# Optimization experiments

Measured on AMD Instinct MI355X. Metric: run time of the kernel, lower is better.

The kernel has to match this reference:

```python
import jax, jax.numpy as jnp
import numpy as np

N_TOKENS = 1024
D = 768
MAX_SPAN_W = 30
FEAT = 20
FFNN = 1000
TOP_RATIO = 0.4
MAX_TOP_ANT = 50
NUM_GENRES = 7
MAX_TRAIN_SENTS = 11
NEG = -1e9
SPAN_DIM = 2 * D + FEAT + D          # start + end + width feat + head-attn emb = 2324
PAIR_DIM = 3 * SPAN_DIM + 4 * FEAT   # 7052


def _ffnn(x, w1, b1, w2, b2):
    # Linear -> ReLU -> Linear (dropout = identity at eval)
    return jax.nn.relu(x @ w1 + b1) @ w2 + b2


def bucket_distance(d):
    # coref-hoi log-space distance bucketing into 10 buckets
    logspace = jnp.floor(jnp.log2(jnp.maximum(d, 1).astype(jnp.float32))).astype(d.dtype) + 3
    return jnp.clip(jnp.where(d <= 4, d, logspace), 0, 9)


def setup_inputs() -> dict:
    key = jax.random.key(0)
    ks = iter(jax.random.split(key, 40))
    rn = lambda shape: jax.random.normal(next(ks), shape, jnp.float32) * 0.02
    return dict(
        token_embs=jax.random.normal(next(ks), (N_TOKENS, D), jnp.float32),
        speaker_ids=jax.random.randint(next(ks), (N_TOKENS,), 0, 10),
        sentence_map=jnp.sort(jax.random.randint(next(ks), (N_TOKENS,), 0, 64)),
        token_seg_ids=jnp.sort(jax.random.randint(next(ks), (N_TOKENS,), 0, 8)),
        genre=3,
        emb_span_width=rn((MAX_SPAN_W, FEAT)),
        emb_span_width_prior=rn((MAX_SPAN_W, FEAT)),
        w_ment_attn=rn((D, 1)), b_ment_attn=jnp.zeros((1,), jnp.float32),
        w_span1=rn((SPAN_DIM, FFNN)), b_span1=jnp.zeros((FFNN,), jnp.float32),
        w_span2=rn((FFNN, 1)), b_span2=jnp.zeros((1,), jnp.float32),
        w_width1=rn((FEAT, FFNN)), b_width1=jnp.zeros((FFNN,), jnp.float32),
        w_width2=rn((FFNN, 1)), b_width2=jnp.zeros((1,), jnp.float32),
        w_biaffine=rn((SPAN_DIM, SPAN_DIM + 1)),
        emb_ant_dist_prior=rn((10, FEAT)),
        w_antdist=rn((FEAT, 1)), b_antdist=jnp.zeros((1,), jnp.float32),
        emb_same_speaker=rn((2, FEAT)),
        emb_genre=rn((NUM_GENRES, FEAT)),
        emb_seg_dist=rn((MAX_TRAIN_SENTS, FEAT)),
        emb_top_ant_dist=rn((10, FEAT)),
        w_pair1=rn((PAIR_DIM, FFNN)), b_pair1=jnp.zeros((FFNN,), jnp.float32),
        w_pair2=rn((FFNN, 1)), b_pair2=jnp.zeros((1,), jnp.float32),
    )


def _forward(token_embs, speaker_ids, sentence_map, token_seg_ids, genre,
             emb_span_width, emb_span_width_prior, w_ment_attn, b_ment_attn,
             w_span1, b_span1, w_span2, b_span2,
             w_width1, b_width1, w_width2, b_width2,
             w_biaffine, emb_ant_dist_prior, w_antdist, b_antdist,
             emb_same_speaker, emb_genre, emb_seg_dist, emb_top_ant_dist,
             w_pair1, b_pair1, w_pair2, b_pair2):
    n = token_embs.shape[0]
    widths = jnp.arange(MAX_SPAN_W)
    starts = jnp.repeat(jnp.arange(n)[:, None], MAX_SPAN_W, axis=1)   # [n, W]
    ends = starts + widths
    ends_c = jnp.minimum(ends, n - 1)
    # candidate valid if it fits in the doc and stays within one sentence
    valid = (ends < n) & (sentence_map[starts] == sentence_map[ends_c])
    starts = starts.reshape(-1)
    ends = ends_c.reshape(-1)
    valid = valid.reshape(-1)
    width_idx = jnp.broadcast_to(widths, (n, MAX_SPAN_W)).reshape(-1)  # [n*W]

    # --- candidate span embeddings ---
    start_emb = token_embs[starts]          # [C, D]
    end_emb = token_embs[ends]              # [C, D]
    width_emb = emb_span_width[width_idx]   # [C, FEAT]
    token_attn = (token_embs @ w_ment_attn + b_ment_attn)[:, 0]        # [n]
    doc = jnp.arange(n)
    span_tok_mask = (starts[:, None] <= doc) & (doc <= ends[:, None])  # [C, n]
    attn = jax.nn.softmax(jnp.where(span_tok_mask, token_attn[None, :], NEG), axis=-1)
    head_emb = attn @ token_embs            # [C, D]
    cand_emb = jnp.concatenate([start_emb, end_emb, width_emb, head_emb], axis=-1)

    # --- mention scores (span emb score + width prior score) ---
    ment = _ffnn(cand_emb, w_span1, b_span1, w_span2, b_span2)[:, 0]
    width_prior = _ffnn(emb_span_width_prior, w_width1, b_width1, w_width2, b_width2)[:, 0]
    ment = jnp.where(valid, ment + width_prior[width_idx], NEG)

    # --- top-span pruning (padded candidates carry -inf scores) ---
    n_top = int(TOP_RATIO * n)
    _, top_idx = jax.lax.top_k(ment, n_top)
    top_idx = jnp.sort(top_idx)             # flat idx = start*W + width -> (start, end) order
    top_starts = starts[top_idx]
    top_ends = ends[top_idx]
    top_emb = cand_emb[top_idx]             # [T, SPAN_DIM]
    top_ment = ment[top_idx]

    # --- coarse antecedent scoring: mention sums + biaffine + distance prior ---
    y = jnp.concatenate([top_emb, jnp.ones((n_top, 1), top_emb.dtype)], axis=-1)  # bias_y
    biaff = jnp.einsum('xi,ij,yj->xy', top_emb, w_biaffine, y)
    offsets = jnp.arange(n_top)[:, None] - jnp.arange(n_top)[None, :]
    ant_mask = offsets >= 1
    dist_prior = (emb_ant_dist_prior @ w_antdist + b_antdist)[:, 0]    # [10]
    coarse = (top_ment[:, None] + top_ment[None, :] + biaff
              + jnp.where(ant_mask, 0.0, NEG)
              + dist_prior[bucket_distance(jnp.maximum(offsets, 0))])

    # --- top-k antecedent pruning ---
    k = min(MAX_TOP_ANT, n_top)
    top_ant_coarse, top_ant_idx = jax.lax.top_k(coarse, k)             # [T, k]
    top_ant_mask = jnp.take_along_axis(ant_mask, top_ant_idx, axis=1)
    top_ant_offsets = jnp.take_along_axis(offsets, top_ant_idx, axis=1)

    # --- pairwise features ---
    top_speaker = speaker_ids[top_starts]
    same_speaker = (top_speaker[:, None] == top_speaker[top_ant_idx]).astype(jnp.int32)
    same_speaker_emb = emb_same_speaker[same_speaker]                  # [T, k, FEAT]
    genre_emb = jnp.broadcast_to(emb_genre[genre], (n_top, k, FEAT))
    top_seg = token_seg_ids[top_starts]
    seg_dist = jnp.clip(top_seg[:, None] - top_seg[top_ant_idx], 0, MAX_TRAIN_SENTS - 1)
    seg_dist_emb = emb_seg_dist[seg_dist]
    ant_dist_emb = emb_top_ant_dist[bucket_distance(jnp.maximum(top_ant_offsets, 0))]
    feat = jnp.concatenate([same_speaker_emb, genre_emb, seg_dist_emb, ant_dist_emb], axis=-1)

    # --- fine (slow) coref scoring over pair embeddings ---
    tgt = top_emb[top_ant_idx]                                         # [T, k, SPAN_DIM]
    src = jnp.broadcast_to(top_emb[:, None], tgt.shape)
    pair = jnp.concatenate([src, tgt, src * tgt, feat], axis=-1)       # [T, k, PAIR_DIM]
    slow = _ffnn(pair, w_pair1, b_pair1, w_pair2, b_pair2)[..., 0]
    ant_scores = jnp.where(top_ant_mask, slow + top_ant_coarse, NEG)
    final = jnp.concatenate([jnp.zeros((n_top, 1), ant_scores.dtype), ant_scores], axis=-1)
    return top_starts, top_ends, top_ant_idx, final


def reference(token_embs, speaker_ids, sentence_map, token_seg_ids, genre,
              emb_span_width, emb_span_width_prior, w_ment_attn, b_ment_attn,
              w_span1, b_span1, w_span2, b_span2,
              w_width1, b_width1, w_width2, b_width2,
              w_biaffine, emb_ant_dist_prior, w_antdist, b_antdist,
              emb_same_speaker, emb_genre, emb_seg_dist, emb_top_ant_dist,
              w_pair1, b_pair1, w_pair2, b_pair2):
    return _forward(token_embs, speaker_ids, sentence_map, token_seg_ids, genre,
                    emb_span_width, emb_span_width_prior, w_ment_attn, b_ment_attn,
                    w_span1, b_span1, w_span2, b_span2,
                    w_width1, b_width1, w_width2, b_width2,
                    w_biaffine, emb_ant_dist_prior, w_antdist, b_antdist,
                    emb_same_speaker, emb_genre, emb_seg_dist, emb_top_ant_dist,
                    w_pair1, b_pair1, w_pair2, b_pair2)
```

## Files before the change

### kernel.cpp

```cpp
#include <hip/hip_runtime.h>
#include <math.h>

#define NEGF (-1e9f)

constexpr int NT = 1024;
constexpr int D  = 768;
constexpr int SW = 30;
constexpr int NC = NT * SW;
constexpr int FT = 20;
constexpr int FF = 1000;
constexpr int TOPN = 409;
constexpr int KA = 50;
constexpr int SD = 2 * D + FT + D;
constexpr int MP = TOPN * KA;
constexpr int KP = 2336;
constexpr int NKT = KP / 32;

typedef short short8 __attribute__((ext_vector_type(8)));
typedef float f32x4 __attribute__((ext_vector_type(4)));

constexpr size_t al8(size_t x) { return (x + 7) & ~(size_t)7; }
constexpr size_t O_TOKATT = 0;
constexpr size_t O_WPS    = al8(O_TOKATT + 1024);
constexpr size_t O_DPR    = al8(O_WPS + 32);
constexpr size_t O_MENT   = al8(O_DPR + 16);
constexpr size_t O_TIDX   = al8(O_MENT + NC);
constexpr size_t O_TST    = al8(O_TIDX + 512);
constexpr size_t O_TEN    = al8(O_TST + 512);
constexpr size_t O_TME    = al8(O_TEN + 512);
constexpr size_t O_TEMB   = al8(O_TME + 512);
constexpr size_t O_TMPB   = al8(O_TEMB + (size_t)TOPN * SD);
constexpr size_t O_COARSE = al8(O_TMPB + (size_t)TOPN * (SD + 1));
constexpr size_t O_ANTI   = al8(O_COARSE + (size_t)TOPN * TOPN);
constexpr size_t O_ANTC   = al8(O_ANTI + 20480);
constexpr size_t O_SLOW   = al8(O_ANTC + 20480);
constexpr size_t O_E      = al8(O_SLOW + 20480);
constexpr size_t O_E2W    = al8(O_E + (size_t)NT * 3072);
constexpr size_t O_PALL   = al8(O_E2W + 30 * 1024);
constexpr size_t O_HST    = al8(O_PALL + 24 * 1024);
constexpr size_t O_TEMBH  = al8(O_HST + (size_t)512 * 2048);
constexpr size_t O_W1ST   = al8(O_TEMBH + (size_t)512 * KP / 2);
constexpr size_t O_W1P    = al8(O_W1ST + (size_t)2048 * KP / 2);

__device__ __forceinline__ unsigned int f2sort(float f) {
    unsigned int u = __float_as_uint(f);
    return (u & 0x80000000u) ? ~u : (u | 0x80000000u);
}
__device__ __forceinline__ int bucket_dist(int d) {
    if (d <= 4) return d;
    return min(34 - __clz(d), 9);
}
__device__ __forceinline__ unsigned short f2bf(float f) {
    unsigned u = __float_as_uint(f);
    unsigned r = (u + 0x7fffu + ((u >> 16) & 1u)) >> 16;
    return (unsigned short)r;
}
__device__ __forceinline__ float bf2f(unsigned short s) {
    return __uint_as_float(((unsigned)s) << 16);
}

__global__ void k_init(const float* b_p2, float* slow) {
    int i = blockIdx.x * 256 + threadIdx.x;
    if (i < MP) slow[i] = b_p2[0];
}

__global__ void k_zero(float* p, int n) {
    int i = blockIdx.x * 256 + threadIdx.x;
    if (i < n) p[i] = 0.f;
}
__global__ void k_zero4(float* p, int n4) {
    int i = blockIdx.x * 256 + threadIdx.x;
    if (i < n4) ((float4*)p)[i] = make_float4(0.f, 0.f, 0.f, 0.f);
}

__global__ void k_tokatt(const float* emb, const float* w, const float* b, float* out) {
    int wave = threadIdx.x >> 6, lane = threadIdx.x & 63;
    int tok = blockIdx.x * 4 + wave;
    float s = 0.f;
    for (int d = lane; d < D; d += 64) s += emb[tok * D + d] * w[d];
    for (int o = 32; o; o >>= 1) s += __shfl_down(s, o);
    if (lane == 0) out[tok] = s + b[0];
}

__global__ void k_widthps(const float* e, const float* w1, const float* b1,
                          const float* w2, const float* b2, float* out) {
    int wi = blockIdx.x;
    float acc = 0.f;
    for (int n = threadIdx.x; n < FF; n += 256) {
        float h = b1[n];
        for (int f = 0; f < FT; ++f) h += e[wi * FT + f] * w1[f * FF + n];
        acc += fmaxf(h, 0.f) * w2[n];
    }
    __shared__ float red[256];
    red[threadIdx.x] = acc; __syncthreads();
    for (int s = 128; s; s >>= 1) {
        if (threadIdx.x < s) red[threadIdx.x] += red[threadIdx.x + s];
        __syncthreads();
    }
    if (threadIdx.x == 0) out[wi] = red[0] + b2[0];
}

__global__ void k_distpr(const float* e, const float* w, const float* b, float* out) {
    int d = threadIdx.x;
    if (d < 10) {
        float s = b[0];
        for (int f = 0; f < FT; ++f) s += e[d * FT + f] * w[f];
        out[d] = s;
    }
}

__global__ void k_e2w(const float* ew, const float* w1, float* e2w) {
    int idx = blockIdx.x * 256 + threadIdx.x;
    if (idx >= 30 * 1024) return;
    int wd = idx >> 10, n = idx & 1023;
    float s = 0.f;
    if (n < FF) for (int f = 0; f < FT; ++f) s += ew[wd * FT + f] * w1[(2 * D + f) * FF + n];
    e2w[idx] = s;
}

__global__ void k_prep_pall(const float* w1, const float* b1, const int* genre,
                            const float* e_same, const float* e_genre,
                            const float* e_seg, const float* e_antd, float* pall) {
    int idx = blockIdx.x * 256 + threadIdx.x;
    if (idx >= 24 * 1024) return;
    int r = idx >> 10, n = idx & 1023;
    float s = 0.f;
    if (n < FF) {
        const float* tab; int foff;
        if (r < 2)       { tab = e_same + r * FT;          foff = 0; }
        else if (r == 2) { tab = e_genre + genre[0] * FT;  foff = FT; s = b1[n]; }
        else if (r < 14) { tab = e_seg + (r - 3) * FT;     foff = 2 * FT; }
        else             { tab = e_antd + (r - 14) * FT;   foff = 3 * FT; }
        for (int f = 0; f < FT; ++f) s += tab[f] * w1[(size_t)(3 * SD + foff + f) * FF + n];
    }
    pall[idx] = s;
}

__global__ void k_cvt_temb(const float* temb, unsigned short* tembh) {
    int idx = blockIdx.x * 256 + threadIdx.x;
    if (idx >= 512 * KP) return;
    int t = idx / KP, k = idx % KP;
    float v = (t < TOPN && k < SD) ? temb[(size_t)t * SD + k] : 0.f;
    tembh[idx] = f2bf(v);
}

__global__ void k_cvt_w1(const float* w1, unsigned short* dst, int mode) {
    __shared__ float tile[32][33];
    int kp0 = blockIdx.x * 32;
    int r0  = blockIdx.y * 32;
    int tx = threadIdx.x & 31, ty = threadIdx.x >> 5;
    for (int i = 0; i < 4; ++i) {
        int r = r0 + tx, kp = kp0 + ty + i * 8;
        int c, ro;
        if (mode == 0) { c = r & 1023; ro = (r >> 10) * SD; }
        else           { c = r;        ro = 2 * SD; }
        float v = (c < FF && kp < SD) ? w1[(size_t)(ro + kp) * FF + c] : 0.f;
        tile[ty + i * 8][tx] = v;
    }
    __syncthreads();
    for (int i = 0; i < 4; ++i) {
        int r = r0 + ty + i * 8, kp = kp0 + tx;
        dst[(size_t)r * KP + kp] = f2bf(tile[tx][ty + i * 8]);
    }
}

__global__ __launch_bounds__(256) void k_ment(
    const float* __restrict__ E, const float* __restrict__ e2w,
    const float* __restrict__ tokatt, const int* __restrict__ sentmap,
    const float* __restrict__ b1, const float* __restrict__ w2,
    const float* __restrict__ wps, const float* __restrict__ b_s2, float* ment) {
    int st = blockIdx.x;
    __shared__ float earr[32];
    __shared__ int vmask[32];
    __shared__ float swred[4][32];
    int tid = threadIdx.x;
    if (tid < SW) {
        int en = st + tid;
        bool ok = en < NT;
        earr[tid] = ok ? expf(tokatt[en]) : 0.f;
        vmask[tid] = ok && (sentmap[st] == sentmap[en]);
    }
    __syncthreads();
    int n4 = tid * 4;
    bool act = n4 < FF;
    float4 Es = {0,0,0,0}, B1 = {0,0,0,0}, W2 = {0,0,0,0};
    if (act) {
        Es = *(const float4*)(E + (size_t)st * 3072 + n4);
        B1 = *(const float4*)(b1 + n4);
        W2 = *(const float4*)(w2 + n4);
    }
    float Ux = 0, Uy = 0, Uz = 0, Uw = 0, S = 0.f;
    float part[SW];
    #pragma unroll
    for (int wd = 0; wd < SW; ++wd) {
        int en = st + wd;
        float p = 0.f;
        if (en < NT) {
            float e = earr[wd]; S += e;
            if (act) {
                float4 Eh = *(const float4*)(E + (size_t)en * 3072 + 2048 + n4);
                Ux += e * Eh.x; Uy += e * Eh.y; Uz += e * Eh.z; Uw += e * Eh.w;
                if (vmask[wd]) {
                    float inv = 1.f / S;
                    float4 Ee = *(const float4*)(E + (size_t)en * 3072 + 1024 + n4);
                    float4 Ww = *(const float4*)(e2w + wd * 1024 + n4);
                    float vx = Es.x + Ee.x + Ww.x + B1.x + Ux * inv;
                    float vy = Es.y + Ee.y + Ww.y + B1.y + Uy * inv;
                    float vz = Es.z + Ee.z + Ww.z + B1.z + Uz * inv;
                    float vw = Es.w + Ee.w + Ww.w + B1.w + Uw * inv;
                    p = fmaxf(vx, 0.f) * W2.x + fmaxf(vy, 0.f) * W2.y
                      + fmaxf(vz, 0.f) * W2.z + fmaxf(vw, 0.f) * W2.w;
                }
            }
        }
        part[wd] = p;
    }
    int lane = tid & 63, wv = tid >> 6;
    #pragma unroll
    for (int wd = 0; wd < SW; ++wd) {
        float r = part[wd];
        r += __shfl_xor(r, 1);  r += __shfl_xor(r, 2);  r += __shfl_xor(r, 4);
        r += __shfl_xor(r, 8);  r += __shfl_xor(r, 16); r += __shfl_xor(r, 32);
        if (lane == 0) swred[wv][wd] = r;
    }
    __syncthreads();
    if (tid < SW) {
        float tot = swred[0][tid] + swred[1][tid] + swred[2][tid] + swred[3][tid];
        ment[st * SW + tid] = vmask[tid] ? (tot + wps[tid] + b_s2[0]) : NEGF;
    }
}

__global__ __launch_bounds__(1024) void k_topk(const float* ment, int* topidx) {
    __shared__ unsigned int hist[256];
    __shared__ unsigned int sc[1024];
    __shared__ unsigned int sh_prefix, sh_needed, sh_run, sh_base2, sh_rune;
    int tid = threadIdx.x;
    if (tid == 0) { sh_prefix = 0; sh_needed = TOPN; }
    for (int r = 3; r >= 0; --r) {
        if (tid < 256) hist[tid] = 0;
        __syncthreads();
        unsigned int pref = sh_prefix;
        for (int c = tid; c < NC; c += 1024) {
            unsigned int u = f2sort(ment[c]);
            bool match = (r == 3) || ((u >> ((r + 1) * 8)) == pref);
            if (match) atomicAdd(&hist[(u >> (r * 8)) & 255u], 1u);
        }
        __syncthreads();
        if (tid == 0) {
            unsigned int need = sh_needed, cum = 0; int sel = 0;
            for (int b = 255; b >= 0; --b) {
                if (cum + hist[b] >= need) { sel = b; sh_needed = need - cum; break; }
                cum += hist[b];
            }
            sh_prefix = (sh_prefix << 8) | (unsigned int)sel;
        }
        __syncthreads();
    }
    unsigned int kth = sh_prefix;
    unsigned int quota = sh_needed;
    if (tid == 0) sh_run = 0;
    __syncthreads();
    for (int base = 0; base < NC; base += 1024) {
        int c = base + tid;
        unsigned int u = f2sort(ment[c]);
        unsigned int flag = (u > kth) ? 1u : 0u;
        sc[tid] = flag; __syncthreads();
        for (int off = 1; off < 1024; off <<= 1) {
            unsigned int v = (tid >= off) ? sc[tid - off] : 0u;
            __syncthreads();
            sc[tid] += v;
            __syncthreads();
        }
        if (flag) topidx[sh_run + sc[tid] - 1] = c;
        unsigned int tot = sc[1023];
        __syncthreads();
        if (tid == 0) sh_run += tot;
        __syncthreads();
    }
    if (tid == 0) { sh_base2 = sh_run; sh_rune = 0; }
    __syncthreads();
    for (int base = 0; base < NC; base += 1024) {
        int c = base + tid;
        unsigned int u = f2sort(ment[c]);
        unsigned int flag = (u == kth) ? 1u : 0u;
        sc[tid] = flag; __syncthreads();
        for (int off = 1; off < 1024; off <<= 1) {
            unsigned int v = (tid >= off) ? sc[tid - off] : 0u;
            __syncthreads();
            sc[tid] += v;
            __syncthreads();
        }
        if (flag && (sh_rune + sc[tid] - 1) < quota)
            topidx[sh_base2 + sh_rune + sc[tid] - 1] = c;
        unsigned int tot = sc[1023];
        __syncthreads();
        if (tid == 0) sh_rune += tot;
        __syncthreads();
    }
    __shared__ int arr[512];
    if (tid < 512) arr[tid] = (tid < TOPN) ? topidx[tid] : 0x7fffffff;
    __syncthreads();
    for (int k = 2; k <= 512; k <<= 1) {
        for (int j = k >> 1; j > 0; j >>= 1) {
            if (tid < 512) {
                int i = tid, p = i ^ j;
                if (p > i) {
                    bool asc = ((i & k) == 0);
                    int a = arr[i], b = arr[p];
                    if ((a > b) == asc) { arr[i] = b; arr[p] = a; }
                }
            }
            __syncthreads();
        }
    }
    if (tid < TOPN) topidx[tid] = arr[tid];
}

__global__ void k_gather(const float* emb, const float* wemb, const float* tokatt,
                         const float* ment, const int* topidx,
                         int* tst, int* ten, float* tme, float* temb,
                         float* out_s, float* out_e) {
    int t = blockIdx.x;
    int c = topidx[t];
    int st = c / SW, wd = c % SW;
    int en = min(st + wd, NT - 1);
    int len = en - st + 1;
    __shared__ float p[32];
    if (threadIdx.x == 0) {
        float m = -1e30f;
        for (int j = 0; j < len; ++j) m = fmaxf(m, tokatt[st + j]);
        float s = 0.f;
        for (int j = 0; j < len; ++j) { p[j] = expf(tokatt[st + j] - m); s += p[j]; }
        float inv = 1.f / s;
        for (int j = 0; j < len; ++j) p[j] *= inv;
        tst[t] = st; ten[t] = en; tme[t] = ment[c];
        out_s[t] = (float)st; out_e[t] = (float)en;
    }
    __syncthreads();
    for (int k = threadIdx.x; k < SD; k += 256) {
        float val;
        if (k < D) val = emb[st * D + k];
        else if (k < 2 * D) val = emb[en * D + (k - D)];
        else if (k < 2 * D + FT) val = wemb[wd * FT + (k - 2 * D)];
        else {
            int d = k - 2 * D - FT;
            float a = 0.f;
            for (int j = 0; j < len; ++j) a += p[j] * emb[(st + j) * D + d];
            val = a;
        }
        temb[(size_t)t * SD + k] = val;
    }
}

template<int BT>
__global__ __launch_bounds__(256) void k_sgemm(
    const float* __restrict__ A, const float* __restrict__ B, float* __restrict__ C,
    int M, int N, int K, int lda, int ldb, int ldc, int kch) {
    int m0 = blockIdx.x * 64, n0 = blockIdx.y * 64;
    int kbeg = blockIdx.z * kch;
    int kend = min(K, kbeg + kch);
    __shared__ float As[32][68], Bs[32][68];
    int tid = threadIdx.x, tx = tid & 15, ty = tid >> 4;
    float acc[4][4] = {};
    float ra[8], rb[8];

    auto loadA = [&](int k0) {
        #pragma unroll
        for (int i = 0; i < 8; ++i) {
            int lid = tid + i * 256;
            int rr = lid >> 5, kk = lid & 31;
            int m = m0 + rr, k = k0 + kk;
            ra[i] = (m < M && k < kend) ? A[(size_t)m * lda + k] : 0.f;
        }
    };
    auto loadB = [&](int k0) {
        #pragma unroll
        for (int i = 0; i < 8; ++i) {
            int lid = tid + i * 256;
            if (BT) {
                int y = lid >> 5, kk = lid & 31;
                int n = n0 + y, k = k0 + kk;
                rb[i] = (n < N && k < kend) ? B[(size_t)n * ldb + k] : 0.f;
            } else {
                int rr = lid >> 6, nn = lid & 63;
                int k = k0 + rr, n = n0 + nn;
                rb[i] = (k < kend && n < N) ? B[(size_t)k * ldb + n] : 0.f;
            }
        }
    };

    loadA(kbeg); loadB(kbeg);
    for (int k0 = kbeg; k0 < kend; k0 += 32) {
        __syncthreads();
        float sa[8], sb[8];
        #pragma unroll
        for (int i = 0; i < 8; ++i) { sa[i] = ra[i]; sb[i] = rb[i]; }
        #pragma unroll
        for (int i = 0; i < 8; ++i) {
            int lid = tid + i * 256;
            As[lid & 31][lid >> 5] = sa[i];
            if (BT) Bs[lid & 31][lid >> 5] = sb[i];
            else    Bs[lid >> 6][lid & 63] = sb[i];
        }
        __syncthreads();
        if (k0 + 32 < kend) { loadA(k0 + 32); loadB(k0 + 32); }
        #pragma unroll
        for (int kk = 0; kk < 32; ++kk) {
            float4 a = *(const float4*)&As[kk][ty * 4];
            float4 b = *(const float4*)&Bs[kk][tx * 4];
            acc[0][0] += a.x * b.x; acc[0][1] += a.x * b.y; acc[0][2] += a.x * b.z; acc[0][3] += a.x * b.w;
            acc[1][0] += a.y * b.x; acc[1][1] += a.y * b.y; acc[1][2] += a.y * b.z; acc[1][3] += a.y * b.w;
            acc[2][0] += a.z * b.x; acc[2][1] += a.z * b.y; acc[2][2] += a.z * b.z; acc[2][3] += a.z * b.w;
            acc[3][0] += a.w * b.x; acc[3][1] += a.w * b.y; acc[3][2] += a.w * b.z; acc[3][3] += a.w * b.w;
        }
    }
    #pragma unroll
    for (int i = 0; i < 4; ++i)
        #pragma unroll
        for (int j = 0; j < 4; ++j) {
            int m = m0 + ty * 4 + i, n = n0 + tx * 4 + j;
            if (m < M && n < N) atomicAdd(&C[(size_t)m * ldc + n], acc[i][j]);
        }
}

__global__ void k_initco(const float* tmpb, const float* tme, const float* dpr, float* coarse) {
    int idx = blockIdx.x * 256 + threadIdx.x;
    if (idx >= TOPN * TOPN) return;
    int x = idx / TOPN, y = idx - x * TOPN;
    int off = x - y;
    coarse[idx] = tmpb[(size_t)x * (SD + 1) + SD] + tme[x] + tme[y]
                + ((off >= 1) ? 0.f : NEGF) + dpr[bucket_dist(max(off, 0))];
}

__global__ __launch_bounds__(256) void k_topant(const float* coarse, int* anti,
                                                float* antc, float* out_ai) {
    int x = blockIdx.x;
    int tid = threadIdx.x;
    __shared__ float vals[512];
    __shared__ unsigned long long red[256];
    vals[tid] = (tid < TOPN) ? coarse[(size_t)x * TOPN + tid] : -INFINITY;
    vals[tid + 256] = (tid + 256 < TOPN) ? coarse[(size_t)x * TOPN + tid + 256] : -INFINITY;
    __syncthreads();
    for (int j = 0; j < KA; ++j) {
        unsigned long long best = 0ull;
        for (int h = 0; h < 2; ++h) {
            int y = tid + h * 256;
            unsigned long long p = ((unsigned long long)f2sort(vals[y]) << 32)
                                 | (unsigned long long)(0xFFFFFFFFu - (unsigned int)y);
            if (p > best) best = p;
        }
        red[tid] = best; __syncthreads();
        for (int s = 128; s; s >>= 1) {
            if (tid < s) { if (red[tid + s] > red[tid]) red[tid] = red[tid + s]; }
            __syncthreads();
        }
        if (tid == 0) {
            unsigned long long r = red[0];
            int y = (int)(0xFFFFFFFFu - (unsigned int)(r & 0xFFFFFFFFu));
            anti[x * KA + j] = y;
            antc[x * KA + j] = vals[y];
            out_ai[x * KA + j] = (float)y;
            vals[y] = -INFINITY;
        }
        __syncthreads();
    }
}

template<int MODE>
__global__ __launch_bounds__(256) void k_mm(
    const unsigned short* __restrict__ tembh, const unsigned short* __restrict__ w1t,
    const int* __restrict__ anti, const int* __restrict__ tstv,
    const int* __restrict__ spk, const int* __restrict__ seg,
    const float* __restrict__ Hst, const float* __restrict__ Pall,
    const float* __restrict__ w2, float* __restrict__ outp) {
    __shared__ unsigned short As[128 * 40];
    __shared__ unsigned short Bs[128 * 40];
    const int tid = threadIdx.x;
    const int m0 = blockIdx.x * 128, n0 = blockIdx.y * 128;
    const int l = tid & 63, wv = tid >> 6, wr = wv >> 1, wc = wv & 1;
    const int r = tid >> 1, h = tid & 1;

    const unsigned short *pa0, *pa1;
    bool za = false;
    if (MODE == 0) {
        pa0 = tembh + (size_t)(m0 + r) * KP + h * 16;
        pa1 = pa0;
    } else {
        int m = m0 + r;
        if (m < MP) {
            int t = m / KA; int a = anti[m];
            pa0 = tembh + (size_t)t * KP + h * 16;
            pa1 = tembh + (size_t)a * KP + h * 16;
        } else { za = true; pa0 = tembh; pa1 = tembh; }
    }
    const unsigned short* pb = w1t + (size_t)(n0 + r) * KP + h * 16;
    unsigned short* awr = As + r * 40 + h * 16;
    unsigned short* bwr = Bs + r * 40 + h * 16;

    short8 ra0, ra1, rb0, rb1, rc0, rc1;
    ra0 = *(const short8*)(pa0); ra1 = *(const short8*)(pa0 + 8);
    if (MODE == 1) { rb0 = *(const short8*)(pa1); rb1 = *(const short8*)(pa1 + 8); }
    rc0 = *(const short8*)(pb);  rc1 = *(const short8*)(pb + 8);

    f32x4 acc[4][4];
    #pragma unroll
    for (int i = 0; i < 4; ++i)
        #pragma unroll
        for (int j = 0; j < 4; ++j) acc[i][j] = (f32x4){0.f, 0.f, 0.f, 0.f};

    for (int kt = 0; kt < NKT; ++kt) {
        __syncthreads();
        short8 wa0, wa1;
        if (MODE == 0) { wa0 = ra0; wa1 = ra1; }
        else {
            #pragma unroll
            for (int e = 0; e < 8; ++e) {
                float x0 = bf2f((unsigned short)ra0[e]) * bf2f((unsigned short)rb0[e]);
                float x1 = bf2f((unsigned short)ra1[e]) * bf2f((unsigned short)rb1[e]);
                wa0[e] = za ? (short)0 : (short)f2bf(x0);
                wa1[e] = za ? (short)0 : (short)f2bf(x1);
            }
        }
        *(short8*)(awr) = wa0; *(short8*)(awr + 8) = wa1;
        *(short8*)(bwr) = rc0; *(short8*)(bwr + 8) = rc1;
        __syncthreads();
        if (kt + 1 < NKT) {
            int ko = (kt + 1) * 32;
            ra0 = *(const short8*)(pa0 + ko); ra1 = *(const short8*)(pa0 + ko + 8);
            if (MODE == 1) { rb0 = *(const short8*)(pa1 + ko); rb1 = *(const short8*)(pa1 + ko + 8); }
            rc0 = *(const short8*)(pb + ko);  rc1 = *(const short8*)(pb + ko + 8);
        }
        short8 af[4], bfr[4];
        #pragma unroll
        for (int mf = 0; mf < 4; ++mf)
            af[mf] = *(const short8*)(As + (wr * 64 + mf * 16 + (l & 15)) * 40 + (l >> 4) * 8);
        #pragma unroll
        for (int nf = 0; nf < 4; ++nf)
            bfr[nf] = *(const short8*)(Bs + (wc * 64 + nf * 16 + (l & 15)) * 40 + (l >> 4) * 8);
        #pragma unroll
        for (int mf = 0; mf < 4; ++mf)
            #pragma unroll
            for (int nf = 0; nf < 4; ++nf)
                acc[mf][nf] = __builtin_amdgcn_mfma_f32_16x16x32_bf16(af[mf], bfr[nf], acc[mf][nf], 0, 0, 0);
    }

    if (MODE == 0) {
        #pragma unroll
        for (int mf = 0; mf < 4; ++mf)
            #pragma unroll
            for (int nf = 0; nf < 4; ++nf)
                #pragma unroll
                for (int rg = 0; rg < 4; ++rg) {
                    int m = m0 + wr * 64 + mf * 16 + (l >> 4) * 4 + rg;
                    int n = n0 + wc * 64 + nf * 16 + (l & 15);
                    outp[(size_t)m * 2048 + n] = acc[mf][nf][rg];
                }
    } else {
        #pragma unroll
        for (int mf = 0; mf < 4; ++mf) {
            #pragma unroll
            for (int rg = 0; rg < 4; ++rg) {
                int m = m0 + wr * 64 + mf * 16 + (l >> 4) * 4 + rg;
                float ps = 0.f;
                if (m < MP) {
                    int t = m / KA; int a = anti[m];
                    int u1 = tstv[t], u2 = tstv[a];
                    const float* rs = Hst + (size_t)t * 2048;
                    const float* rt = Hst + (size_t)a * 2048 + 1024;
                    const float* q1 = Pall + ((spk[u1] == spk[u2]) ? 1 : 0) * 1024;
                    const float* q2 = Pall + 2 * 1024;
                    int sdv = seg[u1] - seg[u2]; sdv = min(max(sdv, 0), 10);
                    const float* q3 = Pall + (3 + sdv) * 1024;
                    const float* q4 = Pall + (14 + bucket_dist(max(t - a, 0))) * 1024;
                    #pragma unroll
                    for (int nf = 0; nf < 4; ++nf) {
                        int n = n0 + wc * 64 + nf * 16 + (l & 15);
                        if (n < FF) {
                            float v = acc[mf][nf][rg] + rs[n] + rt[n] + q1[n] + q2[n] + q3[n] + q4[n];
                            ps += fmaxf(v, 0.f) * w2[n];
                        }
                    }
                }
                ps += __shfl_xor(ps, 1); ps += __shfl_xor(ps, 2);
                ps += __shfl_xor(ps, 4); ps += __shfl_xor(ps, 8);
                if ((l & 15) == 0 && m < MP) atomicAdd(&outp[m], ps);
            }
        }
    }
}

__global__ void k_final(const int* anti, const float* slow, const float* antc, float* out_f) {
    int t = blockIdx.x, j = threadIdx.x;
    if (j < KA) {
        int a = anti[t * KA + j];
        float sc = (a < t) ? (slow[t * KA + j] + antc[t * KA + j]) : NEGF;
        out_f[t * (KA + 1) + 1 + j] = sc;
    }
    if (j == KA) out_f[t * (KA + 1)] = 0.f;
}

extern "C" void kernel_launch(void* const* d_in, const int* in_sizes, int n_in,
                              void* d_out, int out_size, void* d_ws, size_t ws_size,
                              hipStream_t stream) {
    const float* token_embs = (const float*)d_in[0];
    const int*   speaker    = (const int*)d_in[1];
    const int*   sentmap    = (const int*)d_in[2];
    const int*   segids     = (const int*)d_in[3];
    const int*   genre      = (const int*)d_in[4];
    const float* e_width    = (const float*)d_in[5];
    const float* e_width_pr = (const float*)d_in[6];
    const float* w_matt     = (const float*)d_in[7];
    const float* b_matt     = (const float*)d_in[8];
    const float* w_s1       = (const float*)d_in[9];
    const float* b_s1       = (const float*)d_in[10];
    const float* w_s2       = (const float*)d_in[11];
    const float* b_s2       = (const float*)d_in[12];
    const float* w_w1       = (const float*)d_in[13];
    const float* b_w1       = (const float*)d_in[14];
    const float* w_w2       = (const float*)d_in[15];
    const float* b_w2       = (const float*)d_in[16];
    const float* w_bi       = (const float*)d_in[17];
    const float* e_adp      = (const float*)d_in[18];
    const float* w_ad       = (const float*)d_in[19];
    const float* b_ad       = (const float*)d_in[20];
    const float* e_same     = (const float*)d_in[21];
    const float* e_genre    = (const float*)d_in[22];
    const float* e_seg      = (const float*)d_in[23];
    const float* e_antd     = (const float*)d_in[24];
    const float* w_p1       = (const float*)d_in[25];
    const float* b_p1       = (const float*)d_in[26];
    const float* w_p2       = (const float*)d_in[27];
    const float* b_p2       = (const float*)d_in[28];

    float* F = (float*)d_ws;
    float* tokatt = F + O_TOKATT;
    float* wps    = F + O_WPS;
    float* dpr    = F + O_DPR;
    float* ment   = F + O_MENT;
    int*   tidx   = (int*)(F + O_TIDX);
    int*   tst    = (int*)(F + O_TST);
    int*   ten    = (int*)(F + O_TEN);
    float* tme    = F + O_TME;
    float* temb   = F + O_TEMB;
    float* tmpb   = F + O_TMPB;
    float* coarse = F + O_COARSE;
    int*   anti   = (int*)(F + O_ANTI);
    float* antc   = F + O_ANTC;
    float* slow   = F + O_SLOW;
    float* E      = F + O_E;
    float* e2w    = F + O_E2W;
    float* pall   = F + O_PALL;
    float* hst    = F + O_HST;
    unsigned short* tembh = (unsigned short*)(F + O_TEMBH);
    unsigned short* w1st  = (unsigned short*)(F + O_W1ST);
    unsigned short* w1p   = (unsigned short*)(F + O_W1P);

    float* out    = (float*)d_out;
    float* out_s  = out;
    float* out_e  = out + TOPN;
    float* out_ai = out + 2 * TOPN;
    float* out_f  = out + 2 * TOPN + MP;

    k_init<<<(MP + 255) / 256, 256, 0, stream>>>(b_p2, slow);
    k_cvt_w1<<<dim3(NKT, 64), 256, 0, stream>>>(w_p1, w1st, 0);
    k_cvt_w1<<<dim3(NKT, 32), 256, 0, stream>>>(w_p1, w1p, 1);
    k_prep_pall<<<(24 * 1024 + 255) / 256, 256, 0, stream>>>(w_p1, b_p1, genre,
                                                             e_same, e_genre, e_seg, e_antd, pall);
    k_tokatt<<<NT / 4, 256, 0, stream>>>(token_embs, w_matt, b_matt, tokatt);
    k_widthps<<<SW, 256, 0, stream>>>(e_width_pr, w_w1, b_w1, w_w2, b_w2, wps);
    k_distpr<<<1, 64, 0, stream>>>(e_adp, w_ad, b_ad, dpr);

    k_zero4<<<(NT * 3072 / 4 + 255) / 256, 256, 0, stream>>>(E, NT * 3072 / 4);
    {
        dim3 g(NT / 64, (FF + 63) / 64, 2);
        k_sgemm<0><<<g, 256, 0, stream>>>(token_embs, w_s1,                 E,        NT, FF, D, D, FF, 3072, 384);
        k_sgemm<0><<<g, 256, 0, stream>>>(token_embs, w_s1 + D * FF,        E + 1024, NT, FF, D, D, FF, 3072, 384);
        k_sgemm<0><<<g, 256, 0, stream>>>(token_embs, w_s1 + (2*D+FT) * FF, E + 2048, NT, FF, D, D, FF, 3072, 384);
    }
    k_e2w<<<(30 * 1024 + 255) / 256, 256, 0, stream>>>(e_width, w_s1, e2w);

    k_ment<<<NT, 256, 0, stream>>>(E, e2w, tokatt, sentmap, b_s1, w_s2, wps, b_s2, ment);
    k_topk<<<1, 1024, 0, stream>>>(ment, tidx);
    k_gather<<<TOPN, 256, 0, stream>>>(token_embs, e_width, tokatt, ment, tidx,
                                       tst, ten, tme, temb, out_s, out_e);
    k_cvt_temb<<<(512 * KP + 255) / 256, 256, 0, stream>>>(temb, tembh);

    k_zero<<<(TOPN * (SD + 1) + 255) / 256, 256, 0, stream>>>(tmpb, TOPN * (SD + 1));
    {
        dim3 g((TOPN + 63) / 64, (SD + 1 + 63) / 64, 4);
        k_sgemm<0><<<g, 256, 0, stream>>>(temb, w_bi, tmpb, TOPN, SD + 1, SD, SD, SD + 1, SD + 1, 608);
    }
    k_initco<<<(TOPN * TOPN + 255) / 256, 256, 0, stream>>>(tmpb, tme, dpr, coarse);
    {
        dim3 g((TOPN + 63) / 64, (TOPN + 63) / 64, 8);
        k_sgemm<1><<<g, 256, 0, stream>>>(tmpb, temb, coarse, TOPN, TOPN, SD, SD + 1, SD, TOPN, 320);
    }
    k_topant<<<TOPN, 256, 0, stream>>>(coarse, anti, antc, out_ai);

    k_mm<0><<<dim3(4, 16), 256, 0, stream>>>(tembh, w1st, anti, tst, speaker, segids,
                                             hst, pall, w_p2, hst);
    k_mm<1><<<dim3(160, 8), 256, 0, stream>>>(tembh, w1p, anti, tst, speaker, segids,
                                              hst, pall, w_p2, slow);
    k_final<<<TOPN, 64, 0, stream>>>(anti, slow, antc, out_f);
}
```

Measured before the change: 1.100 ms.

## Precompute pair products, speed up topk compaction and per-warp antecedent selection

When the workspace is large enough, a separate kernel materializes the bf16 elementwise products of each span and its antecedent into a buffer, so the pair GEMM streams a plain A matrix instead of doing gathers and multiplies inside its K loop. The grid is transposed so blocks that share an A tile run close together. Top-k compaction now uses a single blocked prefix scan plus a merge by binary search instead of a chunked scan and a bitonic sort. Antecedent top-50 selection uses one wavefront per row with register shuffles instead of shared-memory reductions. The product buffer costs a large extra write and read of memory, and the old fused path is kept as a fallback.

```diff
diff --git a/kernel.cpp b/kernel.cpp
--- a/kernel.cpp
+++ b/kernel.cpp
@@ -13,8 +13,10 @@
 constexpr int KA = 50;
 constexpr int SD = 2 * D + FT + D;
 constexpr int MP = TOPN * KA;
+constexpr int MPP = 20480;
 constexpr int KP = 2336;
 constexpr int NKT = KP / 32;
+constexpr int CHPR = KP / 8;
 
 typedef short short8 __attribute__((ext_vector_type(8)));
 typedef float f32x4 __attribute__((ext_vector_type(4)));
@@ -34,17 +36,23 @@
 constexpr size_t O_ANTI   = al8(O_COARSE + (size_t)TOPN * TOPN);
 constexpr size_t O_ANTC   = al8(O_ANTI + 20480);
 constexpr size_t O_SLOW   = al8(O_ANTC + 20480);
-constexpr size_t O_E      = al8(O_SLOW + 20480);
-constexpr size_t O_E2W    = al8(O_E + (size_t)NT * 3072);
-constexpr size_t O_PALL   = al8(O_E2W + 30 * 1024);
+constexpr size_t O_PALL   = al8(O_SLOW + 20480);
 constexpr size_t O_HST    = al8(O_PALL + 24 * 1024);
 constexpr size_t O_TEMBH  = al8(O_HST + (size_t)512 * 2048);
 constexpr size_t O_W1ST   = al8(O_TEMBH + (size_t)512 * KP / 2);
 constexpr size_t O_W1P    = al8(O_W1ST + (size_t)2048 * KP / 2);
+constexpr size_t O_E      = al8(O_W1P + (size_t)1024 * KP / 2);
+constexpr size_t O_E2W    = O_E + (size_t)NT * 3072;
+constexpr size_t PRODH_F  = (size_t)MPP * KP / 2;
+constexpr size_t O_END_BIG   = O_E + PRODH_F;
+constexpr size_t O_END_SMALL = O_E2W + 30 * 1024;
 
 __device__ __forceinline__ unsigned int f2sort(float f) {
     unsigned int u = __float_as_uint(f);
     return (u & 0x80000000u) ? ~u : (u | 0x80000000u);
+}
+__device__ __forceinline__ float sort2f(unsigned int s) {
+    return __uint_as_float((s & 0x80000000u) ? (s & 0x7FFFFFFFu) : ~s);
 }
 __device__ __forceinline__ int bucket_dist(int d) {
     if (d <= 4) return d;
@@ -162,6 +170,23 @@
         int r = r0 + ty + i * 8, kp = kp0 + tx;
         dst[(size_t)r * KP + kp] = f2bf(tile[tx][ty + i * 8]);
     }
+}
+
+__global__ void k_prod(const unsigned short* __restrict__ tembh, const int* __restrict__ anti,
+                       unsigned short* __restrict__ prodh) {
+    int idx = blockIdx.x * 256 + threadIdx.x;
+    if (idx >= MP * CHPR) return;
+    int m = idx / CHPR;
+    int ch = idx - m * CHPR;
+    int t = m / KA;
+    int a = anti[m];
+    short8 x = *(const short8*)(tembh + (size_t)t * KP + ch * 8);
+    short8 y = *(const short8*)(tembh + (size_t)a * KP + ch * 8);
+    short8 o;
+    #pragma unroll
+    for (int e = 0; e < 8; ++e)
+        o[e] = (short)f2bf(bf2f((unsigned short)x[e]) * bf2f((unsigned short)y[e]));
+    *(short8*)(prodh + (size_t)m * KP + ch * 8) = o;
 }
 
 __global__ __launch_bounds__(256) void k_ment(
@@ -233,87 +258,79 @@
 __global__ __launch_bounds__(1024) void k_topk(const float* ment, int* topidx) {
     __shared__ unsigned int hist[256];
     __shared__ unsigned int sc[1024];
-    __shared__ unsigned int sh_prefix, sh_needed, sh_run, sh_base2, sh_rune;
+    __shared__ int lA[512], lB[512];
+    __shared__ unsigned int sh_prefix, sh_needed;
     int tid = threadIdx.x;
     if (tid == 0) { sh_prefix = 0; sh_needed = TOPN; }
-    for (int r = 3; r >= 0; --r) {
+    for (int rd = 3; rd >= 0; --rd) {
         if (tid < 256) hist[tid] = 0;
         __syncthreads();
-        unsigned int pref = sh_prefix;
+        unsigned pref = sh_prefix;
         for (int c = tid; c < NC; c += 1024) {
-            unsigned int u = f2sort(ment[c]);
-            bool match = (r == 3) || ((u >> ((r + 1) * 8)) == pref);
-            if (match) atomicAdd(&hist[(u >> (r * 8)) & 255u], 1u);
+            unsigned u = f2sort(ment[c]);
+            bool match = (rd == 3) || ((u >> ((rd + 1) * 8)) == pref);
+            if (match) atomicAdd(&hist[(u >> (rd * 8)) & 255u], 1u);
         }
         __syncthreads();
         if (tid == 0) {
-            unsigned int need = sh_needed, cum = 0; int sel = 0;
+            unsigned need = sh_needed, cum = 0; int sel = 0;
             for (int b = 255; b >= 0; --b) {
                 if (cum + hist[b] >= need) { sel = b; sh_needed = need - cum; break; }
                 cum += hist[b];
             }
-            sh_prefix = (sh_prefix << 8) | (unsigned int)sel;
-        }
-        __syncthreads();
-    }
-    unsigned int kth = sh_prefix;
-    unsigned int quota = sh_needed;
-    if (tid == 0) sh_run = 0;
+            sh_prefix = (sh_prefix << 8) | (unsigned)sel;
+        }
+        __syncthreads();
+    }
+    unsigned kth = sh_prefix;
+    int quota = (int)sh_needed;
+    int base = tid * 30;
+    int cgt = 0, ceq = 0;
+    for (int j = 0; j < 30; ++j) {
+        unsigned uu = f2sort(ment[base + j]);
+        cgt += (uu > kth); ceq += (uu == kth);
+    }
+    sc[tid] = (unsigned)cgt; __syncthreads();
+    for (int off = 1; off < 1024; off <<= 1) {
+        unsigned v = (tid >= off) ? sc[tid - off] : 0u;
+        __syncthreads(); sc[tid] += v; __syncthreads();
+    }
+    int egt = (int)sc[tid] - cgt;
+    int nA = (int)sc[1023];
+    int p = egt;
+    for (int j = 0; j < 30; ++j) {
+        int c = base + j;
+        if (f2sort(ment[c]) > kth) lA[p++] = c;
+    }
     __syncthreads();
-    for (int base = 0; base < NC; base += 1024) {
-        int c = base + tid;
-        unsigned int u = f2sort(ment[c]);
-        unsigned int flag = (u > kth) ? 1u : 0u;
-        sc[tid] = flag; __syncthreads();
-        for (int off = 1; off < 1024; off <<= 1) {
-            unsigned int v = (tid >= off) ? sc[tid - off] : 0u;
-            __syncthreads();
-            sc[tid] += v;
-            __syncthreads();
-        }
-        if (flag) topidx[sh_run + sc[tid] - 1] = c;
-        unsigned int tot = sc[1023];
-        __syncthreads();
-        if (tid == 0) sh_run += tot;
-        __syncthreads();
-    }
-    if (tid == 0) { sh_base2 = sh_run; sh_rune = 0; }
+    sc[tid] = (unsigned)ceq; __syncthreads();
+    for (int off = 1; off < 1024; off <<= 1) {
+        unsigned v = (tid >= off) ? sc[tid - off] : 0u;
+        __syncthreads(); sc[tid] += v; __syncthreads();
+    }
+    int eeq = (int)sc[tid] - ceq;
+    p = eeq;
+    for (int j = 0; j < 30; ++j) {
+        int c = base + j;
+        if (f2sort(ment[c]) == kth) { if (p < quota) lB[p] = c; p++; }
+    }
     __syncthreads();
-    for (int base = 0; base < NC; base += 1024) {
-        int c = base + tid;
-        unsigned int u = f2sort(ment[c]);
-        unsigned int flag = (u == kth) ? 1u : 0u;
-        sc[tid] = flag; __syncthreads();
-        for (int off = 1; off < 1024; off <<= 1) {
-            unsigned int v = (tid >= off) ? sc[tid - off] : 0u;
-            __syncthreads();
-            sc[tid] += v;
-            __syncthreads();
-        }
-        if (flag && (sh_rune + sc[tid] - 1) < quota)
-            topidx[sh_base2 + sh_rune + sc[tid] - 1] = c;
-        unsigned int tot = sc[1023];
-        __syncthreads();
-        if (tid == 0) sh_rune += tot;
-        __syncthreads();
-    }
-    __shared__ int arr[512];
-    if (tid < 512) arr[tid] = (tid < TOPN) ? topidx[tid] : 0x7fffffff;
-    __syncthreads();
-    for (int k = 2; k <= 512; k <<= 1) {
-        for (int j = k >> 1; j > 0; j >>= 1) {
-            if (tid < 512) {
-                int i = tid, p = i ^ j;
-                if (p > i) {
-                    bool asc = ((i & k) == 0);
-                    int a = arr[i], b = arr[p];
-                    if ((a > b) == asc) { arr[i] = b; arr[p] = a; }
-                }
-            }
-            __syncthreads();
-        }
-    }
-    if (tid < TOPN) topidx[tid] = arr[tid];
+    if (tid < TOPN) {
+        int v, rank;
+        if (tid < nA) {
+            v = lA[tid];
+            int lo = 0, hi = quota;
+            while (lo < hi) { int mid = (lo + hi) >> 1; if (lB[mid] < v) lo = mid + 1; else hi = mid; }
+            rank = tid + lo;
+        } else {
+            int j = tid - nA;
+            v = lB[j];
+            int lo = 0, hi = nA;
+            while (lo < hi) { int mid = (lo + hi) >> 1; if (lA[mid] < v) lo = mid + 1; else hi = mid; }
+            rank = j + lo;
+        }
+        topidx[rank] = v;
+    }
 }
 
 __global__ void k_gather(const float* emb, const float* wemb, const float* tokatt,
@@ -434,41 +451,44 @@
 
 __global__ __launch_bounds__(256) void k_topant(const float* coarse, int* anti,
                                                 float* antc, float* out_ai) {
-    int x = blockIdx.x;
-    int tid = threadIdx.x;
-    __shared__ float vals[512];
-    __shared__ unsigned long long red[256];
-    vals[tid] = (tid < TOPN) ? coarse[(size_t)x * TOPN + tid] : -INFINITY;
-    vals[tid + 256] = (tid + 256 < TOPN) ? coarse[(size_t)x * TOPN + tid + 256] : -INFINITY;
-    __syncthreads();
-    for (int j = 0; j < KA; ++j) {
+    int x = blockIdx.x * 4 + (threadIdx.x >> 6);
+    int lane = threadIdx.x & 63;
+    if (x >= TOPN) return;
+    unsigned long long pk[8];
+    #pragma unroll
+    for (int j = 0; j < 8; ++j) {
+        int y = lane + 64 * j;
+        pk[j] = (y < TOPN)
+              ? (((unsigned long long)f2sort(coarse[(size_t)x * TOPN + y]) << 32)
+                 | (unsigned long long)(0xFFFFFFFFu - (unsigned)y))
+              : 0ull;
+    }
+    for (int it = 0; it < KA; ++it) {
         unsigned long long best = 0ull;
-        for (int h = 0; h < 2; ++h) {
-            int y = tid + h * 256;
-            unsigned long long p = ((unsigned long long)f2sort(vals[y]) << 32)
-                                 | (unsigned long long)(0xFFFFFFFFu - (unsigned int)y);
-            if (p > best) best = p;
-        }
-        red[tid] = best; __syncthreads();
-        for (int s = 128; s; s >>= 1) {
-            if (tid < s) { if (red[tid + s] > red[tid]) red[tid] = red[tid + s]; }
-            __syncthreads();
-        }
-        if (tid == 0) {
-            unsigned long long r = red[0];
-            int y = (int)(0xFFFFFFFFu - (unsigned int)(r & 0xFFFFFFFFu));
-            anti[x * KA + j] = y;
-            antc[x * KA + j] = vals[y];
-            out_ai[x * KA + j] = (float)y;
-            vals[y] = -INFINITY;
-        }
-        __syncthreads();
+        #pragma unroll
+        for (int j = 0; j < 8; ++j) if (pk[j] > best) best = pk[j];
+        #pragma unroll
+        for (int o = 32; o; o >>= 1) {
+            unsigned long long q = __shfl_xor(best, o);
+            if (q > best) best = q;
+        }
+        int y = (int)(0xFFFFFFFFu - (unsigned)(best & 0xFFFFFFFFu));
+        if (lane == 0) {
+            anti[x * KA + it] = y;
+            antc[x * KA + it] = sort2f((unsigned)(best >> 32));
+            out_ai[x * KA + it] = (float)y;
+        }
+        if (lane == (y & 63)) {
+            int jc = y >> 6;
+            #pragma unroll
+            for (int j = 0; j < 8; ++j) if (j == jc) pk[j] = 0ull;
+        }
     }
 }
 
 template<int MODE>
-__global__ __launch_bounds__(256) void k_mm(
-    const unsigned short* __restrict__ tembh, const unsigned short* __restrict__ w1t,
+__global__ __launch_bounds__(256) void k_mmp(
+    const unsigned short* __restrict__ Ap, const unsigned short* __restrict__ w1t,
     const int* __restrict__ anti, const int* __restrict__ tstv,
     const int* __restrict__ spk, const int* __restrict__ seg,
     const float* __restrict__ Hst, const float* __restrict__ Pall,
@@ -476,31 +496,18 @@
     __shared__ unsigned short As[128 * 40];
     __shared__ unsigned short Bs[128 * 40];
     const int tid = threadIdx.x;
-    const int m0 = blockIdx.x * 128, n0 = blockIdx.y * 128;
+    const int n0 = blockIdx.x * 128, m0 = blockIdx.y * 128;
     const int l = tid & 63, wv = tid >> 6, wr = wv >> 1, wc = wv & 1;
     const int r = tid >> 1, h = tid & 1;
 
-    const unsigned short *pa0, *pa1;
-    bool za = false;
-    if (MODE == 0) {
-        pa0 = tembh + (size_t)(m0 + r) * KP + h * 16;
-        pa1 = pa0;
-    } else {
-        int m = m0 + r;
-        if (m < MP) {
-            int t = m / KA; int a = anti[m];
-            pa0 = tembh + (size_t)t * KP + h * 16;
-            pa1 = tembh + (size_t)a * KP + h * 16;
-        } else { za = true; pa0 = tembh; pa1 = tembh; }
-    }
+    const unsigned short* pa = Ap + (size_t)(m0 + r) * KP + h * 16;
     const unsigned short* pb = w1t + (size_t)(n0 + r) * KP + h * 16;
     unsigned short* awr = As + r * 40 + h * 16;
     unsigned short* bwr = Bs + r * 40 + h * 16;
 
-    short8 ra0, ra1, rb0, rb1, rc0, rc1;
-    ra0 = *(const short8*)(pa0); ra1 = *(const short8*)(pa0 + 8);
-    if (MODE == 1) { rb0 = *(const short8*)(pa1); rb1 = *(const short8*)(pa1 + 8); }
-    rc0 = *(const short8*)(pb);  rc1 = *(const short8*)(pb + 8);
+    short8 ra0, ra1, rc0, rc1;
+    ra0 = *(const short8*)(pa); ra1 = *(const short8*)(pa + 8);
+    rc0 = *(const short8*)(pb); rc1 = *(const short8*)(pb + 8);
 
     f32x4 acc[4][4];
     #pragma unroll
@@ -510,25 +517,13 @@
 
     for (int kt = 0; kt < NKT; ++kt) {
         __syncthreads();
-        short8 wa0, wa1;
-        if (MODE == 0) { wa0 = ra0; wa1 = ra1; }
-        else {
-            #pragma unroll
-            for (int e = 0; e < 8; ++e) {
-                float x0 = bf2f((unsigned short)ra0[e]) * bf2f((unsigned short)rb0[e]);
-                float x1 = bf2f((unsigned short)ra1[e]) * bf2f((unsigned short)rb1[e]);
-                wa0[e] = za ? (short)0 : (short)f2bf(x0);
-                wa1[e] = za ? (short)0 : (short)f2bf(x1);
-            }
-        }
-        *(short8*)(awr) = wa0; *(short8*)(awr + 8) = wa1;
+        *(short8*)(awr) = ra0; *(short8*)(awr + 8) = ra1;
         *(short8*)(bwr) = rc0; *(short8*)(bwr + 8) = rc1;
         __syncthreads();
         if (kt + 1 < NKT) {
             int ko = (kt + 1) * 32;
-            ra0 = *(const short8*)(pa0 + ko); ra1 = *(const short8*)(pa0 + ko + 8);
-            if (MODE == 1) { rb0 = *(const short8*)(pa1 + ko); rb1 = *(const short8*)(pa1 + ko + 8); }
-            rc0 = *(const short8*)(pb + ko);  rc1 = *(const short8*)(pb + ko + 8);
+            ra0 = *(const short8*)(pa + ko); ra1 = *(const short8*)(pa + ko + 8);
+            rc0 = *(const short8*)(pb + ko); rc1 = *(const short8*)(pb + ko + 8);
         }
         short8 af[4], bfr[4];
         #pragma unroll
@@ -585,6 +580,108 @@
                 ps += __shfl_xor(ps, 4); ps += __shfl_xor(ps, 8);
                 if ((l & 15) == 0 && m < MP) atomicAdd(&outp[m], ps);
             }
+        }
+    }
+}
+
+__global__ __launch_bounds__(256) void k_mm_fly(
+    const unsigned short* __restrict__ tembh, const unsigned short* __restrict__ w1t,
+    const int* __restrict__ anti, const int* __restrict__ tstv,
+    const int* __restrict__ spk, const int* __restrict__ seg,
+    const float* __restrict__ Hst, const float* __restrict__ Pall,
+    const float* __restrict__ w2, float* __restrict__ outp) {
+    __shared__ unsigned short As[128 * 40];
+    __shared__ unsigned short Bs[128 * 40];
+    const int tid = threadIdx.x;
+    const int m0 = blockIdx.x * 128, n0 = blockIdx.y * 128;
+    const int l = tid & 63, wv = tid >> 6, wr = wv >> 1, wc = wv & 1;
+    const int r = tid >> 1, h = tid & 1;
+
+    const unsigned short *pa0, *pa1;
+    bool za = false;
+    {
+        int m = m0 + r;
+        if (m < MP) {
+            int t = m / KA; int a = anti[m];
+            pa0 = tembh + (size_t)t * KP + h * 16;
+            pa1 = tembh + (size_t)a * KP + h * 16;
+        } else { za = true; pa0 = tembh; pa1 = tembh; }
+    }
+    const unsigned short* pb = w1t + (size_t)(n0 + r) * KP + h * 16;
+    unsigned short* awr = As + r * 40 + h * 16;
+    unsigned short* bwr = Bs + r * 40 + h * 16;
+
+    short8 ra0, ra1, rb0, rb1, rc0, rc1;
+    ra0 = *(const short8*)(pa0); ra1 = *(const short8*)(pa0 + 8);
+    rb0 = *(const short8*)(pa1); rb1 = *(const short8*)(pa1 + 8);
+    rc0 = *(const short8*)(pb);  rc1 = *(const short8*)(pb + 8);
+
+    f32x4 acc[4][4];
+    #pragma unroll
+    for (int i = 0; i < 4; ++i)
+        #pragma unroll
+        for (int j = 0; j < 4; ++j) acc[i][j] = (f32x4){0.f, 0.f, 0.f, 0.f};
+
+    for (int kt = 0; kt < NKT; ++kt) {
+        __syncthreads();
+        short8 wa0, wa1;
+        #pragma unroll
+        for (int e = 0; e < 8; ++e) {
+            float x0 = bf2f((unsigned short)ra0[e]) * bf2f((unsigned short)rb0[e]);
+            float x1 = bf2f((unsigned short)ra1[e]) * bf2f((unsigned short)rb1[e]);
+            wa0[e] = za ? (short)0 : (short)f2bf(x0);
+            wa1[e] = za ? (short)0 : (short)f2bf(x1);
+        }
+        *(short8*)(awr) = wa0; *(short8*)(awr + 8) = wa1;
+        *(short8*)(bwr) = rc0; *(short8*)(bwr + 8) = rc1;
+        __syncthreads();
+        if (kt + 1 < NKT) {
+            int ko = (kt + 1) * 32;
+            ra0 = *(const short8*)(pa0 + ko); ra1 = *(const short8*)(pa0 + ko + 8);
+            rb0 = *(const short8*)(pa1 + ko); rb1 = *(const short8*)(pa1 + ko + 8);
+            rc0 = *(const short8*)(pb + ko);  rc1 = *(const short8*)(pb + ko + 8);
+        }
+        short8 af[4], bfr[4];
+        #pragma unroll
+        for (int mf = 0; mf < 4; ++mf)
+            af[mf] = *(const short8*)(As + (wr * 64 + mf * 16 + (l & 15)) * 40 + (l >> 4) * 8);
+        #pragma unroll
+        for (int nf = 0; nf < 4; ++nf)
+            bfr[nf] = *(const short8*)(Bs + (wc * 64 + nf * 16 + (l & 15)) * 40 + (l >> 4) * 8);
+        #pragma unroll
+        for (int mf = 0; mf < 4; ++mf)
+            #pragma unroll
+            for (int nf = 0; nf < 4; ++nf)
+                acc[mf][nf] = __builtin_amdgcn_mfma_f32_16x16x32_bf16(af[mf], bfr[nf], acc[mf][nf], 0, 0, 0);
+    }
+    #pragma unroll
+    for (int mf = 0; mf < 4; ++mf) {
+        #pragma unroll
+        for (int rg = 0; rg < 4; ++rg) {
+            int m = m0 + wr * 64 + mf * 16 + (l >> 4) * 4 + rg;
+            float ps = 0.f;
+            if (m < MP) {
+                int t = m / KA; int a = anti[m];
+                int u1 = tstv[t], u2 = tstv[a];
+                const float* rs = Hst + (size_t)t * 2048;
+                const float* rt = Hst + (size_t)a * 2048 + 1024;
+                const float* q1 = Pall + ((spk[u1] == spk[u2]) ? 1 : 0) * 1024;
+                const float* q2 = Pall + 2 * 1024;
+                int sdv = seg[u1] - seg[u2]; sdv = min(max(sdv, 0), 10);
+                const float* q3 = Pall + (3 + sdv) * 1024;
+                const float* q4 = Pall + (14 + bucket_dist(max(t - a, 0))) * 1024;
+                #pragma unroll
+                for (int nf = 0; nf < 4; ++nf) {
+                    int n = n0 + wc * 64 + nf * 16 + (l & 15);
+                    if (n < FF) {
+                        float v = acc[mf][nf][rg] + rs[n] + rt[n] + q1[n] + q2[n] + q3[n] + q4[n];
+                        ps += fmaxf(v, 0.f) * w2[n];
+                    }
+                }
+            }
+            ps += __shfl_xor(ps, 1); ps += __shfl_xor(ps, 2);
+            ps += __shfl_xor(ps, 4); ps += __shfl_xor(ps, 8);
+            if ((l & 15) == 0 && m < MP) atomicAdd(&outp[m], ps);
         }
     }
 }
@@ -647,13 +744,16 @@
     int*   anti   = (int*)(F + O_ANTI);
     float* antc   = F + O_ANTC;
     float* slow   = F + O_SLOW;
-    float* E      = F + O_E;
-    float* e2w    = F + O_E2W;
     float* pall   = F + O_PALL;
     float* hst    = F + O_HST;
     unsigned short* tembh = (unsigned short*)(F + O_TEMBH);
     unsigned short* w1st  = (unsigned short*)(F + O_W1ST);
     unsigned short* w1p   = (unsigned short*)(F + O_W1P);
+    float* E      = F + O_E;
+    float* e2w    = F + O_E2W;
+    unsigned short* prodh = (unsigned short*)(F + O_E);
+
+    bool big = ws_size >= O_END_BIG * sizeof(float);
 
     float* out    = (float*)d_out;
     float* out_s  = out;
@@ -695,11 +795,17 @@
         dim3 g((TOPN + 63) / 64, (TOPN + 63) / 64, 8);
         k_sgemm<1><<<g, 256, 0, stream>>>(tmpb, temb, coarse, TOPN, TOPN, SD, SD + 1, SD, TOPN, 320);
     }
-    k_topant<<<TOPN, 256, 0, stream>>>(coarse, anti, antc, out_ai);
-
-    k_mm<0><<<dim3(4, 16), 256, 0, stream>>>(tembh, w1st, anti, tst, speaker, segids,
-                                             hst, pall, w_p2, hst);
-    k_mm<1><<<dim3(160, 8), 256, 0, stream>>>(tembh, w1p, anti, tst, speaker, segids,
-                                              hst, pall, w_p2, slow);
+    k_topant<<<(TOPN + 3) / 4, 256, 0, stream>>>(coarse, anti, antc, out_ai);
+
+    k_mmp<0><<<dim3(16, 4), 256, 0, stream>>>(tembh, w1st, anti, tst, speaker, segids,
+                                              hst, pall, w_p2, hst);
+    if (big) {
+        k_prod<<<(MP * CHPR + 255) / 256, 256, 0, stream>>>(tembh, anti, prodh);
+        k_mmp<1><<<dim3(8, 160), 256, 0, stream>>>(prodh, w1p, anti, tst, speaker, segids,
+                                                   hst, pall, w_p2, slow);
+    } else {
+        k_mm_fly<<<dim3(160, 8), 256, 0, stream>>>(tembh, w1p, anti, tst, speaker, segids,
+                                                   hst, pall, w_p2, slow);
+    }
     k_final<<<TOPN, 64, 0, stream>>>(anti, slow, antc, out_f);
 }
```

New measurement: 967.7 us. 1.14x faster.
